# Kernel tuning notes

Hardware: AMD Instinct MI355X
Metric: run time of the kernel (lower is better)

The kernel has to match this reference:

```python
import jax, jax.numpy as jnp
import numpy as np

IOU_THRESHOLD = 0.7


def _pairwise_iou(boxes):
    # boxes: [N, 4] as (y1, x1, y2, x2). Returns [N, N] IoU matrix.
    y1, x1, y2, x2 = boxes[:, 0], boxes[:, 1], boxes[:, 2], boxes[:, 3]
    area = (y2 - y1) * (x2 - x1)  # [N]
    iy1 = jnp.maximum(y1[:, None], y1[None, :])
    ix1 = jnp.maximum(x1[:, None], x1[None, :])
    iy2 = jnp.minimum(y2[:, None], y2[None, :])
    ix2 = jnp.minimum(x2[:, None], x2[None, :])
    ih = jnp.clip(iy2 - iy1, 0.0)
    iw = jnp.clip(ix2 - ix1, 0.0)
    inter = ih * iw
    union = area[:, None] + area[None, :] - inter
    return inter / jnp.maximum(union, 1e-9)


def setup_inputs() -> dict:
    key = jax.random.key(0)
    k1, k2, k3 = jax.random.split(key, 3)
    n = 8192
    img = 1024.0
    # Valid boxes: top-left corner + positive width/height, clipped to image.
    tl = jax.random.uniform(k1, (n, 2), dtype=jnp.float32) * (img - 64.0)
    wh = 16.0 + jax.random.uniform(k2, (n, 2), dtype=jnp.float32) * 192.0
    br = jnp.minimum(tl + wh, img)
    bounding_box = jnp.concatenate([tl, br], axis=1)  # (y1, x1, y2, x2)
    cls_score = jax.random.uniform(k3, (n,), dtype=jnp.float32)
    return {"bounding_box": bounding_box, "cls_score": cls_score}


def reference(bounding_box, cls_score):
    # Sort by score descending.
    idx = jnp.argsort(-cls_score)
    bbox = bounding_box[idx]  # [N, 4]
    # NOTE: the original module suppresses box j if ANY earlier box i (i < j)
    # in score order overlaps it (even if box i was itself suppressed), so
    # there is no sequential dependence and it vectorizes exactly:
    iou = _pairwise_iou(bbox)  # [N, N]
    suppress = jnp.triu(iou > IOU_THRESHOLD, k=1)  # row i suppresses col j, i<j
    keep = ~jnp.any(suppress, axis=0)  # [N] bool
    # Original returns bbox[keep] (dynamic shape); for jit-compatibility we
    # return the sorted boxes with suppressed rows zeroed, plus equal math.
    return bbox * keep[:, None].astype(bbox.dtype)
```

## Files before the change

kernel.cpp:

```cpp
#include <hip/hip_runtime.h>
#include <stdint.h>

#define NBOX 8192


__global__ __launch_bounds__(256) void nms_rank_kernel(
    const float4* __restrict__ bbox, const float* __restrict__ score,
    float4* __restrict__ sbox, uint32_t* __restrict__ flags)
{
    __shared__ uint64_t keys[NBOX];
    const int t = threadIdx.x;
    if (blockIdx.x == 0) flags[t] = 0;

    #pragma unroll
    for (int s = 0; s < NBOX / 256; ++s) {
        int i = t + s * 256;
        uint32_t b = __float_as_uint(score[i]);
        keys[i] = ((uint64_t)(b ^ 0xFFFFFFFFu) << 32) | (uint32_t)i;
    }
    __syncthreads();

    const int e = blockIdx.x * 16 + (t >> 4);
    const int p = t & 15;
    const uint64_t myk = keys[e];
    int cnt = 0;
    #pragma unroll 8
    for (int s = 0; s < NBOX / 16; ++s)
        cnt += (keys[s * 16 + p] < myk) ? 1 : 0;

    cnt += __shfl_down(cnt, 8, 16);
    cnt += __shfl_down(cnt, 4, 16);
    cnt += __shfl_down(cnt, 2, 16);
    cnt += __shfl_down(cnt, 1, 16);

    if (p == 0) sbox[cnt] = bbox[e];
}

__global__ __launch_bounds__(256, 4) void nms_suppress_kernel(
    const float4* __restrict__ sbox, uint32_t* __restrict__ flags)
{
    __shared__ float4 LB[32];
    __shared__ float  LTH[32];

    const int tid = threadIdx.x;
    const int b = (int)blockIdx.x;

    int jb = (int)(sqrtf((float)b * 0.0625f + 0.25f) - 0.5f);
    while (16 * (jb + 1) * (jb + 2) <= b) ++jb;
    while (16 * jb * (jb + 1) > b) --jb;
    const int it = b - 16 * jb * (jb + 1);
    const int ibase = it * 32;
    const int jbase = jb * 1024;

    if (tid < 32) {
        float4 bx = sbox[ibase + tid];
        LB[tid] = bx;
        LTH[tid] = 0.4110f * ((bx.z - bx.x) * (bx.w - bx.y));
    }

    const float4 bj0 = sbox[jbase + tid];
    const float4 bj1 = sbox[jbase + 256 + tid];
    const float4 bj2 = sbox[jbase + 512 + tid];
    const float4 bj3 = sbox[jbase + 768 + tid];
    const float tk0 = 0.4110f * ((bj0.z - bj0.x) * (bj0.w - bj0.y));
    const float tk1 = 0.4110f * ((bj1.z - bj1.x) * (bj1.w - bj1.y));
    const float tk2 = 0.4110f * ((bj2.z - bj2.x) * (bj2.w - bj2.y));
    const float tk3 = 0.4110f * ((bj3.z - bj3.x) * (bj3.w - bj3.y));
    __syncthreads();

    uint32_t c0 = 0, c1 = 0, c2 = 0, c3 = 0;
    #pragma unroll 8
    for (int ii = 31; ii >= 0; --ii) {
        const float4 bi = LB[ii];
        const float tia = LTH[ii];
        {
            float ty1 = fmaxf(bi.x, bj0.x), tx1 = fmaxf(bi.y, bj0.y);
            float ty2 = fminf(bi.z, bj0.z), tx2 = fminf(bi.w, bj0.w);
            float ih = fmaxf(ty2 - ty1, 0.0f), iw = fmaxf(tx2 - tx1, 0.0f);
            c0 = (c0 << 1) | ((ih * iw > tia + tk0) ? 1u : 0u);
        }
        {
            float ty1 = fmaxf(bi.x, bj1.x), tx1 = fmaxf(bi.y, bj1.y);
            float ty2 = fminf(bi.z, bj1.z), tx2 = fminf(bi.w, bj1.w);
            float ih = fmaxf(ty2 - ty1, 0.0f), iw = fmaxf(tx2 - tx1, 0.0f);
            c1 = (c1 << 1) | ((ih * iw > tia + tk1) ? 1u : 0u);
        }
        {
            float ty1 = fmaxf(bi.x, bj2.x), tx1 = fmaxf(bi.y, bj2.y);
            float ty2 = fminf(bi.z, bj2.z), tx2 = fminf(bi.w, bj2.w);
            float ih = fmaxf(ty2 - ty1, 0.0f), iw = fmaxf(tx2 - tx1, 0.0f);
            c2 = (c2 << 1) | ((ih * iw > tia + tk2) ? 1u : 0u);
        }
        {
            float ty1 = fmaxf(bi.x, bj3.x), tx1 = fmaxf(bi.y, bj3.y);
            float ty2 = fminf(bi.z, bj3.z), tx2 = fminf(bi.w, bj3.w);
            float ih = fmaxf(ty2 - ty1, 0.0f), iw = fmaxf(tx2 - tx1, 0.0f);
            c3 = (c3 << 1) | ((ih * iw > tia + tk3) ? 1u : 0u);
        }
    }

    {
        int d0 = jbase + tid - ibase;
        int d1 = d0 + 256, d2 = d0 + 512, d3 = d0 + 768;
        c0 &= (d0 <= 0) ? 0u : ((d0 >= 32) ? ~0u : ((1u << d0) - 1u));
        c1 &= (d1 <= 0) ? 0u : ((d1 >= 32) ? ~0u : ((1u << d1) - 1u));
        c2 &= (d2 <= 0) ? 0u : ((d2 >= 32) ? ~0u : ((1u << d2) - 1u));
        c3 &= (d3 <= 0) ? 0u : ((d3 >= 32) ? ~0u : ((1u << d3) - 1u));
    }

    if (c0 | c1 | c2 | c3) {
        #pragma unroll
        for (int q = 0; q < 4; ++q) {
            uint32_t m = (q == 0) ? c0 : (q == 1) ? c1 : (q == 2) ? c2 : c3;
            if (!m) continue;
            const float4 bj = (q == 0) ? bj0 : (q == 1) ? bj1 : (q == 2) ? bj2 : bj3;
            const float ja = __fmul_rn(__fsub_rn(bj.z, bj.x), __fsub_rn(bj.w, bj.y));
            bool h = false;
            do {
                int k = __builtin_ctz(m); m &= m - 1;
                float4 bi = LB[k];
                float ia = __fmul_rn(__fsub_rn(bi.z, bi.x), __fsub_rn(bi.w, bi.y));
                float ty1 = fmaxf(bi.x, bj.x), tx1 = fmaxf(bi.y, bj.y);
                float ty2 = fminf(bi.z, bj.z), tx2 = fminf(bi.w, bj.w);
                float ih = fmaxf(__fsub_rn(ty2, ty1), 0.0f);
                float iw = fmaxf(__fsub_rn(tx2, tx1), 0.0f);
                float inter = __fmul_rn(ih, iw);
                float un = __fsub_rn(__fadd_rn(ia, ja), inter);
                float iou = inter / fmaxf(un, 1e-9f);
                h |= (iou > 0.7f);
            } while (m);
            if (h) {
                int j = jbase + q * 256 + tid;
                atomicOr(&flags[j >> 5], 1u << (j & 31));
            }
        }
    }
}

__global__ __launch_bounds__(256) void nms_write_kernel(
    const float4* __restrict__ sbox, const uint32_t* __restrict__ flags,
    float4* __restrict__ out)
{
    int j = blockIdx.x * 256 + threadIdx.x;
    bool sup = (flags[j >> 5] >> (j & 31)) & 1u;
    float4 v = sbox[j];
    if (sup) { v.x = 0.0f; v.y = 0.0f; v.z = 0.0f; v.w = 0.0f; }
    out[j] = v;
}

extern "C" void kernel_launch(void* const* d_in, const int* in_sizes, int n_in,
                              void* d_out, int out_size, void* d_ws, size_t ws_size,
                              hipStream_t stream) {
    const float4* bbox  = (const float4*)d_in[0];
    const float*  score = (const float*)d_in[1];
    float4* out = (float4*)d_out;
    float4* sbox = (float4*)d_ws;
    uint32_t* flags = (uint32_t*)((char*)d_ws + NBOX * 16);

    hipLaunchKernelGGL(nms_rank_kernel, dim3(NBOX / 16), dim3(256), 0, stream,
                       bbox, score, sbox, flags);
    hipLaunchKernelGGL(nms_suppress_kernel, dim3(1152), dim3(256), 0, stream,
                       sbox, flags);
    hipLaunchKernelGGL(nms_write_kernel, dim3(NBOX / 256), dim3(256), 0, stream,
                       sbox, flags, out);
}
```

Before: 35.60 us.

## Rank from global scores without LDS and retile suppression to 16x1024

The rank kernel no longer stages all 8192 keys in shared memory. Each wave now ranks 4 elements by streaming score bits from global/L2 and reducing the counts with 64-lane shuffles, which removes the large LDS fill and barrier per block. The suppression kernel switches to 128-thread blocks, each comparing 16 i-boxes against 1024 j-boxes held 8 per thread in registers, with an FMA-based threshold test. The launch grid doubles to cover the triangle. The trade-offs are higher register pressure and redundant global reads in the rank loop.

```diff
diff --git a/kernel.cpp b/kernel.cpp
--- a/kernel.cpp
+++ b/kernel.cpp
@@ -5,123 +5,112 @@
 
 
 __global__ __launch_bounds__(256) void nms_rank_kernel(
-    const float4* __restrict__ bbox, const float* __restrict__ score,
+    const float4* __restrict__ bbox, const uint32_t* __restrict__ sb,
     float4* __restrict__ sbox, uint32_t* __restrict__ flags)
 {
-    __shared__ uint64_t keys[NBOX];
-    const int t = threadIdx.x;
-    if (blockIdx.x == 0) flags[t] = 0;
+    const int tid = threadIdx.x;
+    if (blockIdx.x == 0) flags[tid] = 0;
 
+    const int lane = tid & 63;
+    const int e0 = (int)blockIdx.x * 16 + (tid >> 6) * 4;
+
+    uint32_t b0 = sb[e0 + 0], b1 = sb[e0 + 1], b2 = sb[e0 + 2], b3 = sb[e0 + 3];
+    const uint64_t k0 = ((uint64_t)(~b0) << 32) | (uint32_t)(e0 + 0);
+    const uint64_t k1 = ((uint64_t)(~b1) << 32) | (uint32_t)(e0 + 1);
+    const uint64_t k2 = ((uint64_t)(~b2) << 32) | (uint32_t)(e0 + 2);
+    const uint64_t k3 = ((uint64_t)(~b3) << 32) | (uint32_t)(e0 + 3);
+
+    uint32_t c0 = 0, c1 = 0, c2 = 0, c3 = 0;
+    #pragma unroll 8
+    for (int s = 0; s < 128; ++s) {
+        int i = s * 64 + lane;
+        uint32_t b = sb[i];
+        uint64_t k = ((uint64_t)(~b) << 32) | (uint32_t)i;
+        c0 += (k < k0) ? 1u : 0u;
+        c1 += (k < k1) ? 1u : 0u;
+        c2 += (k < k2) ? 1u : 0u;
+        c3 += (k < k3) ? 1u : 0u;
+    }
     #pragma unroll
-    for (int s = 0; s < NBOX / 256; ++s) {
-        int i = t + s * 256;
-        uint32_t b = __float_as_uint(score[i]);
-        keys[i] = ((uint64_t)(b ^ 0xFFFFFFFFu) << 32) | (uint32_t)i;
+    for (int off = 32; off; off >>= 1) {
+        c0 += __shfl_down(c0, off);
+        c1 += __shfl_down(c1, off);
+        c2 += __shfl_down(c2, off);
+        c3 += __shfl_down(c3, off);
     }
-    __syncthreads();
-
-    const int e = blockIdx.x * 16 + (t >> 4);
-    const int p = t & 15;
-    const uint64_t myk = keys[e];
-    int cnt = 0;
-    #pragma unroll 8
-    for (int s = 0; s < NBOX / 16; ++s)
-        cnt += (keys[s * 16 + p] < myk) ? 1 : 0;
-
-    cnt += __shfl_down(cnt, 8, 16);
-    cnt += __shfl_down(cnt, 4, 16);
-    cnt += __shfl_down(cnt, 2, 16);
-    cnt += __shfl_down(cnt, 1, 16);
-
-    if (p == 0) sbox[cnt] = bbox[e];
+    if (lane == 0) {
+        sbox[c0] = bbox[e0 + 0];
+        sbox[c1] = bbox[e0 + 1];
+        sbox[c2] = bbox[e0 + 2];
+        sbox[c3] = bbox[e0 + 3];
+    }
 }
 
-__global__ __launch_bounds__(256, 4) void nms_suppress_kernel(
+__global__ __launch_bounds__(128, 4) void nms_suppress_kernel(
     const float4* __restrict__ sbox, uint32_t* __restrict__ flags)
 {
-    __shared__ float4 LB[32];
-    __shared__ float  LTH[32];
+    __shared__ float4 LB[16];
+    __shared__ float  LTH[16];
 
     const int tid = threadIdx.x;
     const int b = (int)blockIdx.x;
 
-    int jb = (int)(sqrtf((float)b * 0.0625f + 0.25f) - 0.5f);
-    while (16 * (jb + 1) * (jb + 2) <= b) ++jb;
-    while (16 * jb * (jb + 1) > b) --jb;
-    const int it = b - 16 * jb * (jb + 1);
-    const int ibase = it * 32;
+    int jb = 0;
+    while (32 * (jb + 1) * (jb + 2) <= b) ++jb;
+    const int it = b - 32 * jb * (jb + 1);
+    const int ibase = it * 16;
     const int jbase = jb * 1024;
 
-    if (tid < 32) {
+    if (tid < 16) {
         float4 bx = sbox[ibase + tid];
         LB[tid] = bx;
         LTH[tid] = 0.4110f * ((bx.z - bx.x) * (bx.w - bx.y));
     }
 
-    const float4 bj0 = sbox[jbase + tid];
-    const float4 bj1 = sbox[jbase + 256 + tid];
-    const float4 bj2 = sbox[jbase + 512 + tid];
-    const float4 bj3 = sbox[jbase + 768 + tid];
-    const float tk0 = 0.4110f * ((bj0.z - bj0.x) * (bj0.w - bj0.y));
-    const float tk1 = 0.4110f * ((bj1.z - bj1.x) * (bj1.w - bj1.y));
-    const float tk2 = 0.4110f * ((bj2.z - bj2.x) * (bj2.w - bj2.y));
-    const float tk3 = 0.4110f * ((bj3.z - bj3.x) * (bj3.w - bj3.y));
+    float4 bj[8]; float tk[8];
+    #pragma unroll
+    for (int q = 0; q < 8; ++q) {
+        bj[q] = sbox[jbase + q * 128 + tid];
+        tk[q] = 0.4110f * ((bj[q].z - bj[q].x) * (bj[q].w - bj[q].y));
+    }
     __syncthreads();
 
-    uint32_t c0 = 0, c1 = 0, c2 = 0, c3 = 0;
-    #pragma unroll 8
-    for (int ii = 31; ii >= 0; --ii) {
+    uint32_t c[8] = {0, 0, 0, 0, 0, 0, 0, 0};
+    #pragma unroll
+    for (int ii = 15; ii >= 0; --ii) {
         const float4 bi = LB[ii];
-        const float tia = LTH[ii];
-        {
-            float ty1 = fmaxf(bi.x, bj0.x), tx1 = fmaxf(bi.y, bj0.y);
-            float ty2 = fminf(bi.z, bj0.z), tx2 = fminf(bi.w, bj0.w);
+        const float nta = -LTH[ii];
+        #pragma unroll
+        for (int q = 0; q < 8; ++q) {
+            float ty1 = fmaxf(bi.x, bj[q].x), tx1 = fmaxf(bi.y, bj[q].y);
+            float ty2 = fminf(bi.z, bj[q].z), tx2 = fminf(bi.w, bj[q].w);
             float ih = fmaxf(ty2 - ty1, 0.0f), iw = fmaxf(tx2 - tx1, 0.0f);
-            c0 = (c0 << 1) | ((ih * iw > tia + tk0) ? 1u : 0u);
-        }
-        {
-            float ty1 = fmaxf(bi.x, bj1.x), tx1 = fmaxf(bi.y, bj1.y);
-            float ty2 = fminf(bi.z, bj1.z), tx2 = fminf(bi.w, bj1.w);
-            float ih = fmaxf(ty2 - ty1, 0.0f), iw = fmaxf(tx2 - tx1, 0.0f);
-            c1 = (c1 << 1) | ((ih * iw > tia + tk1) ? 1u : 0u);
-        }
-        {
-            float ty1 = fmaxf(bi.x, bj2.x), tx1 = fmaxf(bi.y, bj2.y);
-            float ty2 = fminf(bi.z, bj2.z), tx2 = fminf(bi.w, bj2.w);
-            float ih = fmaxf(ty2 - ty1, 0.0f), iw = fmaxf(tx2 - tx1, 0.0f);
-            c2 = (c2 << 1) | ((ih * iw > tia + tk2) ? 1u : 0u);
-        }
-        {
-            float ty1 = fmaxf(bi.x, bj3.x), tx1 = fmaxf(bi.y, bj3.y);
-            float ty2 = fminf(bi.z, bj3.z), tx2 = fminf(bi.w, bj3.w);
-            float ih = fmaxf(ty2 - ty1, 0.0f), iw = fmaxf(tx2 - tx1, 0.0f);
-            c3 = (c3 << 1) | ((ih * iw > tia + tk3) ? 1u : 0u);
+            float v = fmaf(ih, iw, nta);
+            c[q] = (c[q] << 1) | ((v > tk[q]) ? 1u : 0u);
         }
     }
 
-    {
-        int d0 = jbase + tid - ibase;
-        int d1 = d0 + 256, d2 = d0 + 512, d3 = d0 + 768;
-        c0 &= (d0 <= 0) ? 0u : ((d0 >= 32) ? ~0u : ((1u << d0) - 1u));
-        c1 &= (d1 <= 0) ? 0u : ((d1 >= 32) ? ~0u : ((1u << d1) - 1u));
-        c2 &= (d2 <= 0) ? 0u : ((d2 >= 32) ? ~0u : ((1u << d2) - 1u));
-        c3 &= (d3 <= 0) ? 0u : ((d3 >= 32) ? ~0u : ((1u << d3) - 1u));
+    const int dbase = jbase + tid - ibase;
+    #pragma unroll
+    for (int q = 0; q < 8; ++q) {
+        int d = dbase + q * 128;
+        c[q] &= (d <= 0) ? 0u : ((d >= 16) ? 0xFFFFu : ((1u << d) - 1u));
     }
 
-    if (c0 | c1 | c2 | c3) {
+    if (c[0] | c[1] | c[2] | c[3] | c[4] | c[5] | c[6] | c[7]) {
         #pragma unroll
-        for (int q = 0; q < 4; ++q) {
-            uint32_t m = (q == 0) ? c0 : (q == 1) ? c1 : (q == 2) ? c2 : c3;
+        for (int q = 0; q < 8; ++q) {
+            uint32_t m = c[q];
             if (!m) continue;
-            const float4 bj = (q == 0) ? bj0 : (q == 1) ? bj1 : (q == 2) ? bj2 : bj3;
-            const float ja = __fmul_rn(__fsub_rn(bj.z, bj.x), __fsub_rn(bj.w, bj.y));
+            const float4 bq = bj[q];
+            const float ja = __fmul_rn(__fsub_rn(bq.z, bq.x), __fsub_rn(bq.w, bq.y));
             bool h = false;
             do {
                 int k = __builtin_ctz(m); m &= m - 1;
                 float4 bi = LB[k];
                 float ia = __fmul_rn(__fsub_rn(bi.z, bi.x), __fsub_rn(bi.w, bi.y));
-                float ty1 = fmaxf(bi.x, bj.x), tx1 = fmaxf(bi.y, bj.y);
-                float ty2 = fminf(bi.z, bj.z), tx2 = fminf(bi.w, bj.w);
+                float ty1 = fmaxf(bi.x, bq.x), tx1 = fmaxf(bi.y, bq.y);
+                float ty2 = fminf(bi.z, bq.z), tx2 = fminf(bi.w, bq.w);
                 float ih = fmaxf(__fsub_rn(ty2, ty1), 0.0f);
                 float iw = fmaxf(__fsub_rn(tx2, tx1), 0.0f);
                 float inter = __fmul_rn(ih, iw);
@@ -130,7 +119,7 @@
                 h |= (iou > 0.7f);
             } while (m);
             if (h) {
-                int j = jbase + q * 256 + tid;
+                int j = jbase + q * 128 + tid;
                 atomicOr(&flags[j >> 5], 1u << (j & 31));
             }
         }
@@ -151,15 +140,15 @@
 extern "C" void kernel_launch(void* const* d_in, const int* in_sizes, int n_in,
                               void* d_out, int out_size, void* d_ws, size_t ws_size,
                               hipStream_t stream) {
-    const float4* bbox  = (const float4*)d_in[0];
-    const float*  score = (const float*)d_in[1];
+    const float4*   bbox  = (const float4*)d_in[0];
+    const uint32_t* sbits = (const uint32_t*)d_in[1];
     float4* out = (float4*)d_out;
     float4* sbox = (float4*)d_ws;
     uint32_t* flags = (uint32_t*)((char*)d_ws + NBOX * 16);
 
     hipLaunchKernelGGL(nms_rank_kernel, dim3(NBOX / 16), dim3(256), 0, stream,
-                       bbox, score, sbox, flags);
-    hipLaunchKernelGGL(nms_suppress_kernel, dim3(1152), dim3(256), 0, stream,
+                       bbox, sbits, sbox, flags);
+    hipLaunchKernelGGL(nms_suppress_kernel, dim3(2304), dim3(128), 0, stream,
                        sbox, flags);
     hipLaunchKernelGGL(nms_write_kernel, dim3(NBOX / 256), dim3(256), 0, stream,
                        sbox, flags, out);
```

After: 55.46 us. 1.56x slower.

## Rank scores from global memory with four elements per wave; fuse prefilter into FMA

Applied to the files above, without the earlier changes.

The rank kernel no longer stages all 8192 score keys in shared memory. Each 64-lane wave now ranks four elements, streaming the scores from global/L2, and reduces the four counts with full-wave shuffles. This removes a 64 KB shared-memory fill and a block barrier from each of 512 blocks, in exchange for repeated global reads of the score array. The suppression prefilter comparison is also rewritten as an FMA against the negated threshold, which saves an add per pair but could flip borderline prefilter decisions through rounding.

```diff
diff --git a/kernel.cpp b/kernel.cpp
--- a/kernel.cpp
+++ b/kernel.cpp
@@ -5,35 +5,45 @@
 
 
 __global__ __launch_bounds__(256) void nms_rank_kernel(
-    const float4* __restrict__ bbox, const float* __restrict__ score,
+    const float4* __restrict__ bbox, const uint32_t* __restrict__ sb,
     float4* __restrict__ sbox, uint32_t* __restrict__ flags)
 {
-    __shared__ uint64_t keys[NBOX];
-    const int t = threadIdx.x;
-    if (blockIdx.x == 0) flags[t] = 0;
+    const int tid = threadIdx.x;
+    if (blockIdx.x == 0) flags[tid] = 0;
 
+    const int lane = tid & 63;
+    const int e0 = (int)blockIdx.x * 16 + (tid >> 6) * 4;
+
+    uint32_t b0 = sb[e0 + 0], b1 = sb[e0 + 1], b2 = sb[e0 + 2], b3 = sb[e0 + 3];
+    const uint64_t k0 = ((uint64_t)(~b0) << 32) | (uint32_t)(e0 + 0);
+    const uint64_t k1 = ((uint64_t)(~b1) << 32) | (uint32_t)(e0 + 1);
+    const uint64_t k2 = ((uint64_t)(~b2) << 32) | (uint32_t)(e0 + 2);
+    const uint64_t k3 = ((uint64_t)(~b3) << 32) | (uint32_t)(e0 + 3);
+
+    uint32_t c0 = 0, c1 = 0, c2 = 0, c3 = 0;
+    #pragma unroll 8
+    for (int s = 0; s < 128; ++s) {
+        int i = s * 64 + lane;
+        uint32_t b = sb[i];
+        uint64_t k = ((uint64_t)(~b) << 32) | (uint32_t)i;
+        c0 += (k < k0) ? 1u : 0u;
+        c1 += (k < k1) ? 1u : 0u;
+        c2 += (k < k2) ? 1u : 0u;
+        c3 += (k < k3) ? 1u : 0u;
+    }
     #pragma unroll
-    for (int s = 0; s < NBOX / 256; ++s) {
-        int i = t + s * 256;
-        uint32_t b = __float_as_uint(score[i]);
-        keys[i] = ((uint64_t)(b ^ 0xFFFFFFFFu) << 32) | (uint32_t)i;
+    for (int off = 32; off; off >>= 1) {
+        c0 += __shfl_down(c0, off);
+        c1 += __shfl_down(c1, off);
+        c2 += __shfl_down(c2, off);
+        c3 += __shfl_down(c3, off);
     }
-    __syncthreads();
-
-    const int e = blockIdx.x * 16 + (t >> 4);
-    const int p = t & 15;
-    const uint64_t myk = keys[e];
-    int cnt = 0;
-    #pragma unroll 8
-    for (int s = 0; s < NBOX / 16; ++s)
-        cnt += (keys[s * 16 + p] < myk) ? 1 : 0;
-
-    cnt += __shfl_down(cnt, 8, 16);
-    cnt += __shfl_down(cnt, 4, 16);
-    cnt += __shfl_down(cnt, 2, 16);
-    cnt += __shfl_down(cnt, 1, 16);
-
-    if (p == 0) sbox[cnt] = bbox[e];
+    if (lane == 0) {
+        sbox[c0] = bbox[e0 + 0];
+        sbox[c1] = bbox[e0 + 1];
+        sbox[c2] = bbox[e0 + 2];
+        sbox[c3] = bbox[e0 + 3];
+    }
 }
 
 __global__ __launch_bounds__(256, 4) void nms_suppress_kernel(
@@ -72,30 +82,30 @@
     #pragma unroll 8
     for (int ii = 31; ii >= 0; --ii) {
         const float4 bi = LB[ii];
-        const float tia = LTH[ii];
+        const float nta = -LTH[ii];
         {
             float ty1 = fmaxf(bi.x, bj0.x), tx1 = fmaxf(bi.y, bj0.y);
             float ty2 = fminf(bi.z, bj0.z), tx2 = fminf(bi.w, bj0.w);
             float ih = fmaxf(ty2 - ty1, 0.0f), iw = fmaxf(tx2 - tx1, 0.0f);
-            c0 = (c0 << 1) | ((ih * iw > tia + tk0) ? 1u : 0u);
+            c0 = (c0 << 1) | ((fmaf(ih, iw, nta) > tk0) ? 1u : 0u);
         }
         {
             float ty1 = fmaxf(bi.x, bj1.x), tx1 = fmaxf(bi.y, bj1.y);
             float ty2 = fminf(bi.z, bj1.z), tx2 = fminf(bi.w, bj1.w);
             float ih = fmaxf(ty2 - ty1, 0.0f), iw = fmaxf(tx2 - tx1, 0.0f);
-            c1 = (c1 << 1) | ((ih * iw > tia + tk1) ? 1u : 0u);
+            c1 = (c1 << 1) | ((fmaf(ih, iw, nta) > tk1) ? 1u : 0u);
         }
         {
             float ty1 = fmaxf(bi.x, bj2.x), tx1 = fmaxf(bi.y, bj2.y);
             float ty2 = fminf(bi.z, bj2.z), tx2 = fminf(bi.w, bj2.w);
             float ih = fmaxf(ty2 - ty1, 0.0f), iw = fmaxf(tx2 - tx1, 0.0f);
-            c2 = (c2 << 1) | ((ih * iw > tia + tk2) ? 1u : 0u);
+            c2 = (c2 << 1) | ((fmaf(ih, iw, nta) > tk2) ? 1u : 0u);
         }
         {
             float ty1 = fmaxf(bi.x, bj3.x), tx1 = fmaxf(bi.y, bj3.y);
             float ty2 = fminf(bi.z, bj3.z), tx2 = fminf(bi.w, bj3.w);
             float ih = fmaxf(ty2 - ty1, 0.0f), iw = fmaxf(tx2 - tx1, 0.0f);
-            c3 = (c3 << 1) | ((ih * iw > tia + tk3) ? 1u : 0u);
+            c3 = (c3 << 1) | ((fmaf(ih, iw, nta) > tk3) ? 1u : 0u);
         }
     }
 
@@ -151,14 +161,14 @@
 extern "C" void kernel_launch(void* const* d_in, const int* in_sizes, int n_in,
                               void* d_out, int out_size, void* d_ws, size_t ws_size,
                               hipStream_t stream) {
-    const float4* bbox  = (const float4*)d_in[0];
-    const float*  score = (const float*)d_in[1];
+    const float4*   bbox  = (const float4*)d_in[0];
+    const uint32_t* sbits = (const uint32_t*)d_in[1];
     float4* out = (float4*)d_out;
     float4* sbox = (float4*)d_ws;
     uint32_t* flags = (uint32_t*)((char*)d_ws + NBOX * 16);
 
     hipLaunchKernelGGL(nms_rank_kernel, dim3(NBOX / 16), dim3(256), 0, stream,
-                       bbox, score, sbox, flags);
+                       bbox, sbits, sbox, flags);
     hipLaunchKernelGGL(nms_suppress_kernel, dim3(1152), dim3(256), 0, stream,
                        sbox, flags);
     hipLaunchKernelGGL(nms_write_kernel, dim3(NBOX / 256), dim3(256), 0, stream,
```

New measurement: 32.65 us. 8.3% less time.
